# Kernel optimization log

Hardware: AMD Instinct MI355X
Metric: run time of the kernel (lower is better)

Reference implementation:

```python
import jax, jax.numpy as jnp
import numpy as np

D_MODEL = 1024
HEAD_SIZE = 64

def setup_inputs() -> dict:
    key = jax.random.key(0)
    ks = jax.random.split(key, 7)
    s = 1.0 / np.sqrt(D_MODEL)
    x = jax.random.normal(ks[0], (4, 4096, D_MODEL), dtype=jnp.float32)
    Wq = jax.random.uniform(ks[1], (D_MODEL, HEAD_SIZE), jnp.float32, -s, s)
    bq = jax.random.uniform(ks[2], (HEAD_SIZE,), jnp.float32, -s, s)
    Wk = jax.random.uniform(ks[3], (D_MODEL, HEAD_SIZE), jnp.float32, -s, s)
    bk = jax.random.uniform(ks[4], (HEAD_SIZE,), jnp.float32, -s, s)
    Wv = jax.random.uniform(ks[5], (D_MODEL, HEAD_SIZE), jnp.float32, -s, s)
    bv = jax.random.uniform(ks[6], (HEAD_SIZE,), jnp.float32, -s, s)
    return {"x": x, "Wq": Wq, "bq": bq, "Wk": Wk, "bk": bk, "Wv": Wv, "bv": bv}

def reference(x, Wq, bq, Wk, bk, Wv, bv):
    # x: [B, S, D]; projections to [B, S, H]
    Q = jnp.einsum('bsd,dh->bsh', x, Wq) + bq
    K = jnp.einsum('bsd,dh->bsh', x, Wk) + bk
    V = jnp.einsum('bsd,dh->bsh', x, Wv) + bv
    scores = jnp.einsum('bqh,bkh->bqk', Q, K) / jnp.sqrt(jnp.float32(HEAD_SIZE))
    attn = jax.nn.softmax(scores, axis=-1)  # [B, S, S]
    return jnp.einsum('bqk,bkh->bqh', attn, V)
```

## Files before the change

### kernel.cpp

```cpp
#include <hip/hip_runtime.h>
#include <hip/hip_bf16.h>


#define S_LEN 4096
#define D_MODEL 1024

typedef __attribute__((ext_vector_type(8))) short bf16x8;
typedef __attribute__((ext_vector_type(4))) float f32x4;
typedef __attribute__((ext_vector_type(16))) float f32x16;

__device__ inline short f2bf(float f) {
    union { float f; unsigned u; } v;
    v.f = f;
    unsigned r = v.u + 0x7fffu + ((v.u >> 16) & 1u);
    return (short)(r >> 16);
}

__device__ inline unsigned cvt_pk(float lo, float hi) {
    unsigned r;
    asm("v_cvt_pk_bf16_f32 %0, %1, %2" : "=v"(r) : "v"(lo), "v"(hi));
    return r;
}

__device__ inline void pl32swap(unsigned& a, unsigned& b) {
    asm("v_permlane32_swap_b32 %0, %1" : "+v"(a), "+v"(b));
}

__device__ inline f32x16 fzero16() {
    f32x16 z;
#pragma unroll
    for (int i = 0; i < 16; ++i) z[i] = 0.f;
    return z;
}

__device__ inline void gload_lds16(const void* g, void* l) {
    __builtin_amdgcn_global_load_lds((const __attribute__((address_space(1))) void*)g,
                                     (__attribute__((address_space(3))) void*)l, 16, 0, 0);
}

__global__ void prep_w(const float* __restrict__ Wq, const float* __restrict__ Wk,
                       const float* __restrict__ Wv, short* __restrict__ WtF) {
    int idx = blockIdx.x * 256 + threadIdx.x;
    int j = idx & 7;
    int lane = (idx >> 3) & 63;
    int f = idx >> 9;
    int ntg = f % 12;
    int kb = f / 12;
    int k = (kb >> 1) * 64 + (kb & 1) * 32 + (lane >> 4) * 8 + j;
    int c = ntg * 16 + (lane & 15);
    const float* W = (c < 64) ? Wq : (c < 128 ? Wk : Wv);
    WtF[idx] = f2bf(W[k * 64 + (c & 63)]);
}

__launch_bounds__(512)
__global__ void proj_kernel(const float* __restrict__ x, const short* __restrict__ WtF,
                            const float* __restrict__ bq, const float* __restrict__ bk,
                            const float* __restrict__ bv,
                            short* __restrict__ Qb, short* __restrict__ Kb,
                            short* __restrict__ Vt) {
    __shared__ __align__(16) char smem[81920];
    const float CEXP = 0.18033688011112042f;
    int w = threadIdx.x >> 6;
    int lane = threadIdx.x & 63;
    int g = lane >> 4, ln = lane & 15;
    int rt = w >> 1, nh = w & 1;
    int rowbase = blockIdx.x * 64;

    char* xbuf = smem;
    char* wbuf = smem + 32768;
    const char* xB = (const char*)x;
    const char* WtB = (const char*)WtF;

    auto stageX = [&](int buf, int bkt) {
#pragma unroll
        for (int i = 0; i < 2; ++i) {
            int od = w * 2048 + i * 1024 + lane * 16;
            int row = od >> 8, col = od & 255;
            const char* src = xB + (size_t)(rowbase + row) * 4096 + bkt * 256
                              + (col ^ ((row & 7) << 5));
            gload_lds16(src, xbuf + buf * 16384 + w * 2048 + i * 1024);
        }
    };
    auto stageW = [&](int buf, int bkt) {
#pragma unroll
        for (int i = 0; i < 3; ++i) {
            const char* src = WtB + (size_t)bkt * 24576 + w * 3072 + i * 1024 + lane * 16;
            gload_lds16(src, wbuf + buf * 24576 + w * 3072 + i * 1024);
        }
    };

    f32x4 acc[6];
#pragma unroll
    for (int i = 0; i < 6; ++i) acc[i] = (f32x4){0.f, 0.f, 0.f, 0.f};

    stageX(0, 0);
    stageW(0, 0);

    int arow = rt * 16 + ln;
    int aswz = (arow & 7) << 5;

#pragma unroll 1
    for (int t = 0; t < 16; ++t) {
        asm volatile("s_waitcnt vmcnt(0)" ::: "memory");
        __builtin_amdgcn_s_barrier();
        __builtin_amdgcn_sched_barrier(0);
        if (t < 15) {
            stageX((t + 1) & 1, t + 1);
            stageW((t + 1) & 1, t + 1);
        }
        const char* xc = xbuf + (t & 1) * 16384;
        const char* wc = wbuf + (t & 1) * 24576;

#pragma unroll
        for (int kk = 0; kk < 2; ++kk) {
            int cb = (kk * 128 + g * 32) ^ aswz;
            f32x4 X0 = *(const f32x4*)(xc + arow * 256 + cb);
            f32x4 X1 = *(const f32x4*)(xc + arow * 256 + cb + 16);
            union { bf16x8 v; unsigned u[4]; } A;
            A.u[0] = cvt_pk(X0[0], X0[1]);
            A.u[1] = cvt_pk(X0[2], X0[3]);
            A.u[2] = cvt_pk(X1[0], X1[1]);
            A.u[3] = cvt_pk(X1[2], X1[3]);
#pragma unroll
            for (int nt = 0; nt < 6; ++nt) {
                int fr = kk * 12 + nh * 6 + nt;
                bf16x8 bfr = *(const bf16x8*)(wc + fr * 1024 + lane * 16);
                acc[nt] = __builtin_amdgcn_mfma_f32_16x16x32_bf16(A.v, bfr, acc[nt], 0, 0, 0);
            }
        }
    }

    __syncthreads();
    short* vsm = (short*)smem;
#pragma unroll
    for (int nt = 0; nt < 6; ++nt) {
        int ntg = nh * 6 + nt;
        int c = ntg * 16 + ln;
        int proj = ntg >> 2;
        int h = c & 63;
        float bias = (proj == 0 ? bq : (proj == 1 ? bk : bv))[h];
#pragma unroll
        for (int r = 0; r < 4; ++r) {
            int srow = rowbase + rt * 16 + g * 4 + r;
            float v = acc[nt][r] + bias;
            if (proj == 0) v *= CEXP;
            short hv = f2bf(v);
            if (proj == 0) {
                Qb[(size_t)srow * 64 + h] = hv;
            } else if (proj == 1) {
                Kb[(size_t)srow * 64 + h] = hv;
            } else {
                vsm[h * 72 + rt * 16 + g * 4 + r] = hv;
            }
        }
    }
    __syncthreads();
    {
        int t = threadIdx.x;
        int h = t >> 3, c = t & 7;
        bf16x8 val = *(const bf16x8*)&vsm[h * 72 + c * 8];
        int bb = rowbase >> 12;
        int sg = (rowbase & 4095) + c * 8;
        *(bf16x8*)(Vt + ((size_t)(bb * 64 + h) << 12) + sg) = val;
    }
}

__launch_bounds__(512)
__global__ void attn_kernel(const short* __restrict__ Qb, const short* __restrict__ Kb,
                            const short* __restrict__ Vt, float* __restrict__ out) {
    __shared__ __align__(16) char smraw[131072];
    __shared__ float lsm[256];
    int lane = threadIdx.x & 63;
    int w = threadIdx.x >> 6;
    int l31 = lane & 31, hi = lane >> 5;
    int sp = w >> 1, qt = w & 1;

    int bid = blockIdx.x;
    int sb = (bid & 7) * 32 + (bid >> 3);
    int b = sb >> 6, qs = sb & 63;
    size_t qrow0 = ((size_t)b << 12) + (size_t)qs * 64;

    char* base = smraw + sp * 32768;
    char* kbuf = base;
    char* vbuf = base + 16384;

    const char* KB = (const char*)(Kb + (((size_t)b << 12) + sp * 1024) * 64);
    const char* VB = (const char*)Vt + (((size_t)b * 64) << 13) + (size_t)sp * 2048;

    auto stageT = [&](int buf, int t) {
        if (qt == 0) {
            char* dst = kbuf + buf * 8192;
#pragma unroll
            for (int i = 0; i < 8; ++i) {
                int od = i * 1024 + lane * 16;
                int row = od >> 7, colb = od & 127;
                const char* src = KB + (size_t)(t * 64 + row) * 128 + (colb ^ ((row & 7) << 4));
                gload_lds16(src, dst + i * 1024);
            }
        } else {
            char* dst = vbuf + buf * 8192;
#pragma unroll
            for (int i = 0; i < 8; ++i) {
                int od = i * 1024 + lane * 16;
                int row = od >> 7, colb = od & 127;
                const char* src = VB + (size_t)row * 8192 + t * 128 + (colb ^ ((row & 7) << 4));
                gload_lds16(src, dst + i * 1024);
            }
        }
    };

    bf16x8 qf[4];
    {
        const short* qp = Qb + (qrow0 + qt * 32 + l31) * 64 + hi * 8;
#pragma unroll
        for (int ks = 0; ks < 4; ++ks) qf[ks] = *(const bf16x8*)(qp + ks * 16);
    }

    f32x16 oacc0 = fzero16(), oacc1 = fzero16();
    float lacc[16];
#pragma unroll
    for (int r = 0; r < 16; ++r) lacc[r] = 0.f;

    int swz = (l31 & 7) << 4;
    stageT(0, 0);

#pragma unroll 1
    for (int t = 0; t < 16; ++t) {
        asm volatile("s_waitcnt vmcnt(0)" ::: "memory");
        __builtin_amdgcn_s_barrier();
        __builtin_amdgcn_sched_barrier(0);
        if (t < 15) stageT((t + 1) & 1, t + 1);

        const char* kc = kbuf + (t & 1) * 8192;
        const char* vc = vbuf + (t & 1) * 8192;

        bf16x8 kf[8];
#pragma unroll
        for (int kt = 0; kt < 2; ++kt)
#pragma unroll
            for (int ks = 0; ks < 4; ++ks)
                kf[kt * 4 + ks] = *(const bf16x8*)(kc + (kt * 32 + l31) * 128
                                                  + ((ks * 32 + hi * 16) ^ swz));
        f32x16 s0 = fzero16(), s1 = fzero16();
#pragma unroll
        for (int ks = 0; ks < 4; ++ks) {
            s0 = __builtin_amdgcn_mfma_f32_32x32x16_bf16(kf[ks], qf[ks], s0, 0, 0, 0);
            s1 = __builtin_amdgcn_mfma_f32_32x32x16_bf16(kf[4 + ks], qf[ks], s1, 0, 0, 0);
        }

        bf16x8 vf[8];
#pragma unroll
        for (int ht = 0; ht < 2; ++ht)
#pragma unroll
            for (int kk = 0; kk < 4; ++kk)
                vf[ht * 4 + kk] = *(const bf16x8*)(vc + (ht * 32 + l31) * 128
                                                   + ((kk * 32 + hi * 16) ^ swz));

        float p0[16], p1[16];
#pragma unroll
        for (int r = 0; r < 16; ++r) p0[r] = exp2f(s0[r]);
#pragma unroll
        for (int r = 0; r < 16; ++r) p1[r] = exp2f(s1[r]);
#pragma unroll
        for (int r = 0; r < 16; ++r) lacc[r] += p0[r] + p1[r];

        union { unsigned u[4]; bf16x8 v; } t00, t01, t10, t11;
        {
            unsigned D[8];
#pragma unroll
            for (int dw = 0; dw < 8; ++dw) D[dw] = cvt_pk(p0[2 * dw], p0[2 * dw + 1]);
            pl32swap(D[0], D[2]); pl32swap(D[1], D[3]);
            pl32swap(D[4], D[6]); pl32swap(D[5], D[7]);
            t00.u[0] = D[0]; t00.u[1] = D[1]; t00.u[2] = D[2]; t00.u[3] = D[3];
            t01.u[0] = D[4]; t01.u[1] = D[5]; t01.u[2] = D[6]; t01.u[3] = D[7];
        }
        {
            unsigned D[8];
#pragma unroll
            for (int dw = 0; dw < 8; ++dw) D[dw] = cvt_pk(p1[2 * dw], p1[2 * dw + 1]);
            pl32swap(D[0], D[2]); pl32swap(D[1], D[3]);
            pl32swap(D[4], D[6]); pl32swap(D[5], D[7]);
            t10.u[0] = D[0]; t10.u[1] = D[1]; t10.u[2] = D[2]; t10.u[3] = D[3];
            t11.u[0] = D[4]; t11.u[1] = D[5]; t11.u[2] = D[6]; t11.u[3] = D[7];
        }

        oacc0 = __builtin_amdgcn_mfma_f32_32x32x16_bf16(vf[0], t00.v, oacc0, 0, 0, 0);
        oacc1 = __builtin_amdgcn_mfma_f32_32x32x16_bf16(vf[4], t00.v, oacc1, 0, 0, 0);
        oacc0 = __builtin_amdgcn_mfma_f32_32x32x16_bf16(vf[1], t01.v, oacc0, 0, 0, 0);
        oacc1 = __builtin_amdgcn_mfma_f32_32x32x16_bf16(vf[5], t01.v, oacc1, 0, 0, 0);
        oacc0 = __builtin_amdgcn_mfma_f32_32x32x16_bf16(vf[2], t10.v, oacc0, 0, 0, 0);
        oacc1 = __builtin_amdgcn_mfma_f32_32x32x16_bf16(vf[6], t10.v, oacc1, 0, 0, 0);
        oacc0 = __builtin_amdgcn_mfma_f32_32x32x16_bf16(vf[3], t11.v, oacc0, 0, 0, 0);
        oacc1 = __builtin_amdgcn_mfma_f32_32x32x16_bf16(vf[7], t11.v, oacc1, 0, 0, 0);
    }

    float lfin;
    {
        float lt[8];
#pragma unroll
        for (int r = 0; r < 8; ++r) lt[r] = lacc[r] + lacc[r + 8];
#pragma unroll
        for (int st = 4; st >= 1; st >>= 1)
#pragma unroll
            for (int r = 0; r < 4; ++r)
                if (r < st) lt[r] += lt[r + st];
        lfin = lt[0] + __shfl_xor(lt[0], 32);
    }

    __syncthreads();
    float* osm = (float*)smraw;
    {
        float* ow = osm + (size_t)(w * 32 + l31) * 68;
#pragma unroll
        for (int r = 0; r < 16; ++r) {
            int h = (r & 3) + 8 * (r >> 2) + 4 * hi;
            ow[h] = oacc0[r];
            ow[32 + h] = oacc1[r];
        }
        if (hi == 0) lsm[w * 32 + l31] = lfin;
    }
    __syncthreads();
    {
        int tq = threadIdx.x >> 3, hb = (threadIdx.x & 7) * 8;
        int qt2 = tq >> 5, ql = tq & 31;
        f32x4 oa = (f32x4){0.f, 0.f, 0.f, 0.f}, ob = (f32x4){0.f, 0.f, 0.f, 0.f};
        float lsum = 0.f;
#pragma unroll
        for (int sp2 = 0; sp2 < 4; ++sp2) {
            int w2 = sp2 * 2 + qt2;
            lsum += lsm[w2 * 32 + ql];
            const float* src = osm + (size_t)(w2 * 32 + ql) * 68 + hb;
            f32x4 x0 = *(const f32x4*)src;
            f32x4 x1 = *(const f32x4*)(src + 4);
#pragma unroll
            for (int j = 0; j < 4; ++j) { oa[j] += x0[j]; ob[j] += x1[j]; }
        }
        float inv = 1.f / lsum;
        f32x4 r0, r1;
#pragma unroll
        for (int j = 0; j < 4; ++j) { r0[j] = oa[j] * inv; r1[j] = ob[j] * inv; }
        float* op = out + (qrow0 + tq) * 64 + hb;
        *(f32x4*)op = r0;
        *(f32x4*)(op + 4) = r1;
    }
}

extern "C" void kernel_launch(void* const* d_in, const int* in_sizes, int n_in,
                              void* d_out, int out_size, void* d_ws, size_t ws_size,
                              hipStream_t stream) {
    const float* x  = (const float*)d_in[0];
    const float* Wq = (const float*)d_in[1];
    const float* bq = (const float*)d_in[2];
    const float* Wk = (const float*)d_in[3];
    const float* bk = (const float*)d_in[4];
    const float* Wv = (const float*)d_in[5];
    const float* bv = (const float*)d_in[6];

    short* ws = (short*)d_ws;
    short* WtF = ws;
    short* Qb = WtF + 192 * 1024;
    short* Kb = Qb + 16384 * 64;
    short* Vt = Kb + 16384 * 64;

    prep_w<<<768, 256, 0, stream>>>(Wq, Wk, Wv, WtF);
    proj_kernel<<<256, 512, 0, stream>>>(x, WtF, bq, bk, bv, Qb, Kb, Vt);
    attn_kernel<<<256, 512, 0, stream>>>(Qb, Kb, Vt, (float*)d_out);
}
```

Measured before the change: 60.08 us.

## Halve projection row tile to 32 rows and deepen x prefetch pipeline

The projection kernel now processes 32 rows per block instead of 64, launching 512 blocks so more CUs get work, with each wave computing 3 output column tiles instead of 6. The x tile uses a triple-buffered ring prefetched two steps ahead, and the wait is relaxed to vmcnt(1) so the next x load can stay in flight while computing. The trade-off is that the weight tile is reloaded twice as often in total, and the V transpose now uses narrower 8-byte stores.

Measured after the change: 59.35 us. No clear change (-1.2%).

```diff
diff --git a/kernel.cpp b/kernel.cpp
--- a/kernel.cpp
+++ b/kernel.cpp
@@ -58,28 +58,25 @@
                             const float* __restrict__ bv,
                             short* __restrict__ Qb, short* __restrict__ Kb,
                             short* __restrict__ Vt) {
-    __shared__ __align__(16) char smem[81920];
+    __shared__ __align__(16) char smem[73728];
     const float CEXP = 0.18033688011112042f;
     int w = threadIdx.x >> 6;
     int lane = threadIdx.x & 63;
     int g = lane >> 4, ln = lane & 15;
-    int rt = w >> 1, nh = w & 1;
-    int rowbase = blockIdx.x * 64;
+    int rt = w >> 2, nh = w & 3;
+    int rowbase = blockIdx.x * 32;
 
     char* xbuf = smem;
-    char* wbuf = smem + 32768;
+    char* wbuf = smem + 24576;
     const char* xB = (const char*)x;
     const char* WtB = (const char*)WtF;
 
     auto stageX = [&](int buf, int bkt) {
-#pragma unroll
-        for (int i = 0; i < 2; ++i) {
-            int od = w * 2048 + i * 1024 + lane * 16;
-            int row = od >> 8, col = od & 255;
-            const char* src = xB + (size_t)(rowbase + row) * 4096 + bkt * 256
-                              + (col ^ ((row & 7) << 5));
-            gload_lds16(src, xbuf + buf * 16384 + w * 2048 + i * 1024);
-        }
+        int od = w * 1024 + lane * 16;
+        int row = od >> 8, col = od & 255;
+        const char* src = xB + (size_t)(rowbase + row) * 4096 + bkt * 256
+                          + (col ^ ((row & 7) << 5));
+        gload_lds16(src, xbuf + buf * 8192 + w * 1024);
     };
     auto stageW = [&](int buf, int bkt) {
 #pragma unroll
@@ -89,26 +86,31 @@
         }
     };
 
-    f32x4 acc[6];
-#pragma unroll
-    for (int i = 0; i < 6; ++i) acc[i] = (f32x4){0.f, 0.f, 0.f, 0.f};
+    f32x4 acc[3];
+#pragma unroll
+    for (int i = 0; i < 3; ++i) acc[i] = (f32x4){0.f, 0.f, 0.f, 0.f};
 
     stageX(0, 0);
     stageW(0, 0);
+    stageX(1, 1);
 
     int arow = rt * 16 + ln;
     int aswz = (arow & 7) << 5;
 
 #pragma unroll 1
     for (int t = 0; t < 16; ++t) {
-        asm volatile("s_waitcnt vmcnt(0)" ::: "memory");
+        asm volatile("s_waitcnt vmcnt(1)" ::: "memory");
         __builtin_amdgcn_s_barrier();
         __builtin_amdgcn_sched_barrier(0);
-        if (t < 15) {
-            stageX((t + 1) & 1, t + 1);
-            stageW((t + 1) & 1, t + 1);
-        }
-        const char* xc = xbuf + (t & 1) * 16384;
+        {
+            int tn1 = t + 1 > 15 ? 15 : t + 1;
+            int tn2 = t + 2 > 15 ? 15 : t + 2;
+            stageW((t + 1) & 1, tn1);
+            int xs = t + 2; while (xs >= 3) xs -= 3;
+            stageX(xs, tn2);
+        }
+        int xj = t; while (xj >= 3) xj -= 3;
+        const char* xc = xbuf + xj * 8192;
         const char* wc = wbuf + (t & 1) * 24576;
 
 #pragma unroll
@@ -122,10 +124,10 @@
             A.u[2] = cvt_pk(X1[0], X1[1]);
             A.u[3] = cvt_pk(X1[2], X1[3]);
 #pragma unroll
-            for (int nt = 0; nt < 6; ++nt) {
-                int fr = kk * 12 + nh * 6 + nt;
+            for (int j = 0; j < 3; ++j) {
+                int fr = kk * 12 + nh * 3 + j;
                 bf16x8 bfr = *(const bf16x8*)(wc + fr * 1024 + lane * 16);
-                acc[nt] = __builtin_amdgcn_mfma_f32_16x16x32_bf16(A.v, bfr, acc[nt], 0, 0, 0);
+                acc[j] = __builtin_amdgcn_mfma_f32_16x16x32_bf16(A.v, bfr, acc[j], 0, 0, 0);
             }
         }
     }
@@ -133,8 +135,8 @@
     __syncthreads();
     short* vsm = (short*)smem;
 #pragma unroll
-    for (int nt = 0; nt < 6; ++nt) {
-        int ntg = nh * 6 + nt;
+    for (int j = 0; j < 3; ++j) {
+        int ntg = nh * 3 + j;
         int c = ntg * 16 + ln;
         int proj = ntg >> 2;
         int h = c & 63;
@@ -142,7 +144,7 @@
 #pragma unroll
         for (int r = 0; r < 4; ++r) {
             int srow = rowbase + rt * 16 + g * 4 + r;
-            float v = acc[nt][r] + bias;
+            float v = acc[j][r] + bias;
             if (proj == 0) v *= CEXP;
             short hv = f2bf(v);
             if (proj == 0) {
@@ -150,7 +152,7 @@
             } else if (proj == 1) {
                 Kb[(size_t)srow * 64 + h] = hv;
             } else {
-                vsm[h * 72 + rt * 16 + g * 4 + r] = hv;
+                vsm[h * 36 + rt * 16 + g * 4 + r] = hv;
             }
         }
     }
@@ -158,10 +160,10 @@
     {
         int t = threadIdx.x;
         int h = t >> 3, c = t & 7;
-        bf16x8 val = *(const bf16x8*)&vsm[h * 72 + c * 8];
+        uint2 val = *(const uint2*)(vsm + h * 36 + c * 4);
         int bb = rowbase >> 12;
-        int sg = (rowbase & 4095) + c * 8;
-        *(bf16x8*)(Vt + ((size_t)(bb * 64 + h) << 12) + sg) = val;
+        int sg = (rowbase & 4095) + c * 4;
+        *(uint2*)(Vt + (((size_t)(bb * 64 + h)) << 12) + sg) = val;
     }
 }
 
@@ -363,6 +365,6 @@
     short* Vt = Kb + 16384 * 64;
 
     prep_w<<<768, 256, 0, stream>>>(Wq, Wk, Wv, WtF);
-    proj_kernel<<<256, 512, 0, stream>>>(x, WtF, bq, bk, bv, Qb, Kb, Vt);
+    proj_kernel<<<512, 512, 0, stream>>>(x, WtF, bq, bk, bv, Qb, Kb, Vt);
     attn_kernel<<<256, 512, 0, stream>>>(Qb, Kb, Vt, (float*)d_out);
 }
```
